# Performance work log

Measured on AMD Instinct MI355X. Metric: run time of the kernel, lower is better.

The kernel has to match this reference:

```python
import jax, jax.numpy as jnp
import numpy as np

ITEM_NUM = 100000
EMBED = 128
HIDDEN = 256
BETA = 0.5
B = 4096
H = 200

def setup_inputs() -> dict:
    key = jax.random.key(0)
    ks = jax.random.split(key, 7)
    history = jax.random.randint(ks[0], (B, H), 0, ITEM_NUM)
    target = jax.random.randint(ks[1], (B,), 0, ITEM_NUM)
    embed_history = jax.random.normal(ks[2], (ITEM_NUM, EMBED), dtype=jnp.float32) * 0.01
    embed_target = jax.random.normal(ks[3], (ITEM_NUM, EMBED), dtype=jnp.float32) * 0.01
    # nn.Linear default init: U(-1/sqrt(fan_in), 1/sqrt(fan_in)); biases zeroed by _init_weight_
    lim1 = 1.0 / np.sqrt(EMBED)
    W1 = jax.random.uniform(ks[4], (EMBED, HIDDEN), dtype=jnp.float32, minval=-lim1, maxval=lim1)
    b1 = jnp.zeros((HIDDEN,), dtype=jnp.float32)
    lim2 = 1.0 / np.sqrt(HIDDEN)
    w2 = jax.random.uniform(ks[5], (HIDDEN,), dtype=jnp.float32, minval=-lim2, maxval=lim2)
    return {"history": history, "target": target, "embed_history": embed_history,
            "embed_target": embed_target, "W1": W1, "b1": b1, "w2": w2}

def reference(history, target, embed_history, embed_target, W1, b1, w2):
    hist_e = embed_history[history]            # [B, H, d]
    tgt_e = embed_target[target][:, None, :]   # [B, 1, d]
    x = hist_e * tgt_e                          # [B, H, d]
    a = jnp.einsum('bhk,k->bh', jax.nn.relu(jnp.einsum('bhd,dk->bhk', x, W1) + b1), w2)  # [B, H]
    mask = (history != target[:, None]).astype(a.dtype)  # [B, H]
    exp_A = jnp.exp(a) * mask                  # [B, H]
    denom = jnp.sum(exp_A, axis=-1) ** BETA    # [B], beta-power normalization (not softmax)
    attn = exp_A / denom[:, None]              # [B, H]
    pred = jnp.einsum('bh,bhd,bd->b', attn, hist_e, tgt_e[:, 0, :])  # [B]
    return jax.nn.sigmoid(pred)
```

## Files before the change

kernel.cpp:

```cpp
#include <hip/hip_runtime.h>

#define B_SZ   4096
#define H_SZ   200
#define D_SZ   128
#define N_SZ   256
#define ROWS   (B_SZ * H_SZ)
#define BM     64
#define TPB    8
#define RPB    (BM * TPB)
#define NBLK   (ROWS / RPB)

typedef __attribute__((ext_vector_type(8))) short bf16x8;
typedef __attribute__((ext_vector_type(4))) float f32x4;

__device__ __forceinline__ unsigned short f2bf(float f) {
    unsigned u = __builtin_bit_cast(unsigned, f);
    u += 0x7FFFu + ((u >> 16) & 1u);
    return (unsigned short)(u >> 16);
}
__device__ __forceinline__ float bflo(unsigned d) {
    return __builtin_bit_cast(float, d << 16);
}
__device__ __forceinline__ float bfhi(unsigned d) {
    return __builtin_bit_cast(float, d & 0xFFFF0000u);
}
__device__ __forceinline__ unsigned packtr(float a, float b) {
    return (__builtin_bit_cast(unsigned, a) >> 16) |
           (__builtin_bit_cast(unsigned, b) & 0xFFFF0000u);
}

__global__ __launch_bounds__(256) void cvt_eh(const float* __restrict__ src,
                                              uint4* __restrict__ dst, int n8) {
    int i = blockIdx.x * 256 + threadIdx.x;
    if (i >= n8) return;
    const f32x4* p = (const f32x4*)src + (size_t)i * 2;
    f32x4 a = p[0], b = p[1];
    uint4 o;
    o.x = (unsigned)f2bf(a[0]) | ((unsigned)f2bf(a[1]) << 16);
    o.y = (unsigned)f2bf(a[2]) | ((unsigned)f2bf(a[3]) << 16);
    o.z = (unsigned)f2bf(b[0]) | ((unsigned)f2bf(b[1]) << 16);
    o.w = (unsigned)f2bf(b[2]) | ((unsigned)f2bf(b[3]) << 16);
    dst[i] = o;
}

__global__ __launch_bounds__(256) void cvt_w1(const float* __restrict__ src,
                                              unsigned short* __restrict__ dst) {
    int i = blockIdx.x * 256 + threadIdx.x;
    int n = i >> 7, d = i & 127;
    dst[i] = f2bf(src[d * N_SZ + n]);
}

__global__ __launch_bounds__(512, 4) void nais_main(
    const int* __restrict__ history, const int* __restrict__ target,
    const uint4* __restrict__ eh16, const float* __restrict__ et,
    const unsigned short* __restrict__ w1t, const float* __restrict__ b1,
    const float* __restrict__ w2,
    float* __restrict__ a_out, float* __restrict__ dotd_out)
{
    __shared__ uint4 AbufV[2][BM * 256 / 16];
    __shared__ float apart[2][8][BM];
    __shared__ float tgt_p[4][16][12];
    __shared__ int   tgt_i[4];

    const int tid  = threadIdx.x;
    const int wid  = tid >> 6;
    const int lane = tid & 63;
    const int lo   = lane & 15;
    const int hi   = lane >> 4;
    const int row  = tid >> 3;
    const int seg  = tid & 7;
    const int blk  = blockIdx.x;
    const int b_base = (blk * RPB) / H_SZ;

    if (tid < 4) {
        int bb = b_base + tid;
        tgt_i[tid] = target[bb < B_SZ ? bb : (B_SZ - 1)];
    }
    __syncthreads();
    {
        const int r4 = tid >> 7, d = tid & 127;
        tgt_p[r4][d >> 3][d & 7] = et[(size_t)tgt_i[r4] * D_SZ + d];
    }

    bf16x8 wfrag[4][2];
    #pragma unroll
    for (int ni = 0; ni < 2; ++ni) {
        int n = 32 * wid + 16 * ni + lo;
        #pragma unroll
        for (int ki = 0; ki < 4; ++ki)
            wfrag[ki][ni] = *(const bf16x8*)(w1t + (size_t)n * D_SZ + 32 * ki + 8 * hi);
    }
    const int n0 = 32 * wid + 4 * hi;
    const f32x4 b1a = *(const f32x4*)(b1 + n0);
    const f32x4 b1b = *(const f32x4*)(b1 + n0 + 16);
    const f32x4 w2a = *(const f32x4*)(w2 + n0);
    const f32x4 w2b = *(const f32x4*)(w2 + n0 + 16);

    const int grow0 = blk * RPB + row;
    const int* hrow = history + grow0;
    int ih_nxt = hrow[BM];
    uint4 hq0, hq1;
    {
        const uint4* p = eh16 + (size_t)hrow[0] * 16;
        hq0 = p[seg]; hq1 = p[8 + seg];
    }
    __syncthreads();

    for (int t = 0; t < TPB; ++t) {
        char* Ab = (char*)AbufV[t & 1];
        const int gr    = grow0 + t * BM;
        const int b_loc = gr / H_SZ - b_base;

        {
            const float* tA = &tgt_p[b_loc][seg][0];
            const float* tB = &tgt_p[b_loc][8 + seg][0];
            f32x4 ta0 = *(const f32x4*)tA, ta1 = *(const f32x4*)(tA + 4);
            f32x4 tb0 = *(const f32x4*)tB, tb1 = *(const f32x4*)(tB + 4);
            float tAv[8] = {ta0[0], ta0[1], ta0[2], ta0[3], ta1[0], ta1[1], ta1[2], ta1[3]};
            float tBv[8] = {tb0[0], tb0[1], tb0[2], tb0[3], tb1[0], tb1[1], tb1[2], tb1[3]};
            unsigned h1[4] = {hq0.x, hq0.y, hq0.z, hq0.w};
            unsigned h2[4] = {hq1.x, hq1.y, hq1.z, hq1.w};
            unsigned xp1[4], xp2[4];
            float s = 0.f;
            #pragma unroll
            for (int j = 0; j < 4; ++j) {
                float x0 = bflo(h1[j]) * tAv[2 * j];
                float x1 = bfhi(h1[j]) * tAv[2 * j + 1];
                float y0 = bflo(h2[j]) * tBv[2 * j];
                float y1 = bfhi(h2[j]) * tBv[2 * j + 1];
                s += (x0 + x1) + (y0 + y1);
                xp1[j] = packtr(x0, x1);
                xp2[j] = packtr(y0, y1);
            }
            s += __shfl_xor(s, 1);
            s += __shfl_xor(s, 2);
            s += __shfl_xor(s, 4);
            if (seg == 0) dotd_out[gr] = s;
            const unsigned sw = (unsigned)((row & 7) << 4);
            char* rb = Ab + row * 256;
            *(uint4*)(rb + (((unsigned)(16 * seg)) ^ sw))          = uint4{xp1[0], xp1[1], xp1[2], xp1[3]};
            *(uint4*)(rb + (128u + (((unsigned)(16 * seg)) ^ sw))) = uint4{xp2[0], xp2[1], xp2[2], xp2[3]};
        }
        __syncthreads();

        if (t + 1 < TPB) {
            int ih_cur = ih_nxt;
            if (t + 2 < TPB) ih_nxt = hrow[(t + 2) * BM];
            const uint4* p = eh16 + (size_t)ih_cur * 16;
            hq0 = p[seg]; hq1 = p[8 + seg];
        }

        if (t > 0 && tid < BM) {
            const float* ap = &apart[(t - 1) & 1][0][tid];
            float a = ap[0];
            #pragma unroll
            for (int w = 1; w < 8; ++w) a += ap[w * BM];
            a_out[blk * RPB + (t - 1) * BM + tid] = a;
        }

        #pragma unroll
        for (int mi = 0; mi < 4; ++mi) {
            const int rr = 16 * mi + lo;
            const unsigned swr = (unsigned)((rr & 7) << 4);
            bf16x8 af[4];
            #pragma unroll
            for (int ki = 0; ki < 4; ++ki) {
                unsigned off = ((unsigned)(64 * ki + 16 * hi)) ^ swr;
                af[ki] = *(const bf16x8*)(Ab + rr * 256 + off);
            }
            f32x4 acc0 = b1a;
            f32x4 acc1 = b1b;
            __builtin_amdgcn_s_setprio(1);
            #pragma unroll
            for (int ki = 0; ki < 4; ++ki) {
                acc0 = __builtin_amdgcn_mfma_f32_16x16x32_bf16(wfrag[ki][0], af[ki], acc0, 0, 0, 0);
                acc1 = __builtin_amdgcn_mfma_f32_16x16x32_bf16(wfrag[ki][1], af[ki], acc1, 0, 0, 0);
            }
            __builtin_amdgcn_s_setprio(0);
            float v = fmaxf(acc0[0], 0.f) * w2a[0] + fmaxf(acc1[0], 0.f) * w2b[0];
            v += fmaxf(acc0[1], 0.f) * w2a[1] + fmaxf(acc1[1], 0.f) * w2b[1];
            v += fmaxf(acc0[2], 0.f) * w2a[2] + fmaxf(acc1[2], 0.f) * w2b[2];
            v += fmaxf(acc0[3], 0.f) * w2a[3] + fmaxf(acc1[3], 0.f) * w2b[3];
            v += __shfl_xor(v, 16);
            v += __shfl_xor(v, 32);
            if (lane < 16) apart[t & 1][wid][16 * mi + lane] = v;
        }
    }
    __syncthreads();
    if (tid < BM) {
        const float* ap = &apart[(TPB - 1) & 1][0][tid];
        float a = ap[0];
        #pragma unroll
        for (int w = 1; w < 8; ++w) a += ap[w * BM];
        a_out[blk * RPB + (TPB - 1) * BM + tid] = a;
    }
}

__global__ __launch_bounds__(64) void nais_finish(
    const int* __restrict__ history, const int* __restrict__ target,
    const float* __restrict__ a_in, const float* __restrict__ dotd_in,
    float* __restrict__ out)
{
    const int b    = blockIdx.x;
    const int lane = threadIdx.x;
    const int tgt  = target[b];
    float s1 = 0.f, s2 = 0.f;
    for (int h = lane; h < H_SZ; h += 64) {
        int rg = b * H_SZ + h;
        float e = (history[rg] != tgt) ? __expf(a_in[rg]) : 0.f;
        s1 += e;
        s2 += e * dotd_in[rg];
    }
    #pragma unroll
    for (int o = 1; o < 64; o <<= 1) {
        s1 += __shfl_xor(s1, o);
        s2 += __shfl_xor(s2, o);
    }
    if (lane == 0) {
        float pred = s2 / sqrtf(s1);
        out[b] = 1.f / (1.f + __expf(-pred));
    }
}

extern "C" void kernel_launch(void* const* d_in, const int* in_sizes, int n_in,
                              void* d_out, int out_size, void* d_ws, size_t ws_size,
                              hipStream_t stream) {
    const int*   history = (const int*)d_in[0];
    const int*   target  = (const int*)d_in[1];
    const float* eh      = (const float*)d_in[2];
    const float* et      = (const float*)d_in[3];
    const float* W1      = (const float*)d_in[4];
    const float* b1      = (const float*)d_in[5];
    const float* w2      = (const float*)d_in[6];
    float* out = (float*)d_out;

    char* ws = (char*)d_ws;
    uint4*          eh16 = (uint4*)ws;
    unsigned short* w1t  = (unsigned short*)(ws + (size_t)100000 * D_SZ * 2);
    float*          a_ws = (float*)(ws + (size_t)100000 * D_SZ * 2 + N_SZ * D_SZ * 2);
    float*          dotd_ws = a_ws + ROWS;

    const int n8 = 100000 * D_SZ / 8;
    cvt_eh<<<(n8 + 255) / 256, 256, 0, stream>>>(eh, eh16, n8);
    cvt_w1<<<(N_SZ * D_SZ) / 256, 256, 0, stream>>>(W1, w1t);
    nais_main<<<NBLK, 512, 0, stream>>>(history, target, eh16, et, w1t, b1, w2, a_ws, dotd_ws);
    nais_finish<<<B_SZ, 64, 0, stream>>>(history, target, a_ws, dotd_ws, out);
}
```

Before: 101.5 us.

## Switch bf16 path to scaled fp16 with packed multiply and dot2

```diff
diff --git a/kernel.cpp b/kernel.cpp
--- a/kernel.cpp
+++ b/kernel.cpp
@@ -10,23 +10,15 @@
 #define RPB    (BM * TPB)
 #define NBLK   (ROWS / RPB)
 
-typedef __attribute__((ext_vector_type(8))) short bf16x8;
+typedef _Float16 f16;
+typedef __attribute__((ext_vector_type(2))) _Float16 f16x2;
+typedef __attribute__((ext_vector_type(8))) _Float16 f16x8;
 typedef __attribute__((ext_vector_type(4))) float f32x4;
 
-__device__ __forceinline__ unsigned short f2bf(float f) {
-    unsigned u = __builtin_bit_cast(unsigned, f);
-    u += 0x7FFFu + ((u >> 16) & 1u);
-    return (unsigned short)(u >> 16);
-}
-__device__ __forceinline__ float bflo(unsigned d) {
-    return __builtin_bit_cast(float, d << 16);
-}
-__device__ __forceinline__ float bfhi(unsigned d) {
-    return __builtin_bit_cast(float, d & 0xFFFF0000u);
-}
-__device__ __forceinline__ unsigned packtr(float a, float b) {
-    return (__builtin_bit_cast(unsigned, a) >> 16) |
-           (__builtin_bit_cast(unsigned, b) & 0xFFFF0000u);
+union H8 { f16x8 v; f16x2 p[4]; uint4 u; };
+
+__device__ __forceinline__ f16x2 pkrtz(float a, float b) {
+    return __builtin_bit_cast(f16x2, __builtin_amdgcn_cvt_pkrtz(a, b));
 }
 
 __global__ __launch_bounds__(256) void cvt_eh(const float* __restrict__ src,
@@ -36,30 +28,30 @@
     const f32x4* p = (const f32x4*)src + (size_t)i * 2;
     f32x4 a = p[0], b = p[1];
     uint4 o;
-    o.x = (unsigned)f2bf(a[0]) | ((unsigned)f2bf(a[1]) << 16);
-    o.y = (unsigned)f2bf(a[2]) | ((unsigned)f2bf(a[3]) << 16);
-    o.z = (unsigned)f2bf(b[0]) | ((unsigned)f2bf(b[1]) << 16);
-    o.w = (unsigned)f2bf(b[2]) | ((unsigned)f2bf(b[3]) << 16);
+    o.x = __builtin_bit_cast(unsigned, pkrtz(a[0], a[1]));
+    o.y = __builtin_bit_cast(unsigned, pkrtz(a[2], a[3]));
+    o.z = __builtin_bit_cast(unsigned, pkrtz(b[0], b[1]));
+    o.w = __builtin_bit_cast(unsigned, pkrtz(b[2], b[3]));
     dst[i] = o;
 }
 
 __global__ __launch_bounds__(256) void cvt_w1(const float* __restrict__ src,
-                                              unsigned short* __restrict__ dst) {
+                                              f16* __restrict__ dst) {
     int i = blockIdx.x * 256 + threadIdx.x;
     int n = i >> 7, d = i & 127;
-    dst[i] = f2bf(src[d * N_SZ + n]);
+    dst[i] = (f16)(src[d * N_SZ + n] * 0.0625f);
 }
 
 __global__ __launch_bounds__(512, 4) void nais_main(
     const int* __restrict__ history, const int* __restrict__ target,
-    const uint4* __restrict__ eh16, const float* __restrict__ et,
-    const unsigned short* __restrict__ w1t, const float* __restrict__ b1,
+    const uint4* __restrict__ ehh, const float* __restrict__ et,
+    const f16* __restrict__ w1t, const float* __restrict__ b1,
     const float* __restrict__ w2,
     float* __restrict__ a_out, float* __restrict__ dotd_out)
 {
     __shared__ uint4 AbufV[2][BM * 256 / 16];
     __shared__ float apart[2][8][BM];
-    __shared__ float tgt_p[4][16][12];
+    __shared__ f16   tgt_h[4][D_SZ];
     __shared__ int   tgt_i[4];
 
     const int tid  = threadIdx.x;
@@ -77,18 +69,19 @@
         tgt_i[tid] = target[bb < B_SZ ? bb : (B_SZ - 1)];
     }
     __syncthreads();
-    {
-        const int r4 = tid >> 7, d = tid & 127;
-        tgt_p[r4][d >> 3][d & 7] = et[(size_t)tgt_i[r4] * D_SZ + d];
-    }
-
-    bf16x8 wfrag[4][2];
+    if (tid < 256) {
+        const int r4 = tid >> 6, j = (tid & 63) * 2;
+        const float* src = et + (size_t)tgt_i[r4] * D_SZ + j;
+        ((f16x2*)tgt_h)[tid] = pkrtz(src[0] * 16.f, src[1] * 16.f);
+    }
+
+    f16x8 wfrag[4][2];
     #pragma unroll
     for (int ni = 0; ni < 2; ++ni) {
         int n = 32 * wid + 16 * ni + lo;
         #pragma unroll
         for (int ki = 0; ki < 4; ++ki)
-            wfrag[ki][ni] = *(const bf16x8*)(w1t + (size_t)n * D_SZ + 32 * ki + 8 * hi);
+            wfrag[ki][ni] = *(const f16x8*)(w1t + (size_t)n * D_SZ + 32 * ki + 8 * hi);
     }
     const int n0 = 32 * wid + 4 * hi;
     const f32x4 b1a = *(const f32x4*)(b1 + n0);
@@ -98,55 +91,49 @@
 
     const int grow0 = blk * RPB + row;
     const int* hrow = history + grow0;
+    int ih_cur = hrow[0];
     int ih_nxt = hrow[BM];
     uint4 hq0, hq1;
     {
-        const uint4* p = eh16 + (size_t)hrow[0] * 16;
+        const uint4* p = ehh + (size_t)ih_cur * 16;
         hq0 = p[seg]; hq1 = p[8 + seg];
     }
+    int b_loc = grow0 / H_SZ - b_base;
+    int rem   = grow0 - (b_loc + b_base) * H_SZ;
     __syncthreads();
 
     for (int t = 0; t < TPB; ++t) {
         char* Ab = (char*)AbufV[t & 1];
-        const int gr    = grow0 + t * BM;
-        const int b_loc = gr / H_SZ - b_base;
+        const int gr = grow0 + t * BM;
 
         {
-            const float* tA = &tgt_p[b_loc][seg][0];
-            const float* tB = &tgt_p[b_loc][8 + seg][0];
-            f32x4 ta0 = *(const f32x4*)tA, ta1 = *(const f32x4*)(tA + 4);
-            f32x4 tb0 = *(const f32x4*)tB, tb1 = *(const f32x4*)(tB + 4);
-            float tAv[8] = {ta0[0], ta0[1], ta0[2], ta0[3], ta1[0], ta1[1], ta1[2], ta1[3]};
-            float tBv[8] = {tb0[0], tb0[1], tb0[2], tb0[3], tb1[0], tb1[1], tb1[2], tb1[3]};
-            unsigned h1[4] = {hq0.x, hq0.y, hq0.z, hq0.w};
-            unsigned h2[4] = {hq1.x, hq1.y, hq1.z, hq1.w};
-            unsigned xp1[4], xp2[4];
+            H8 h1, h2, t1, t2, x1, x2;
+            h1.u = hq0; h2.u = hq1;
+            t1.v = *(const f16x8*)&tgt_h[b_loc][8 * seg];
+            t2.v = *(const f16x8*)&tgt_h[b_loc][64 + 8 * seg];
+            x1.v = h1.v * t1.v;
+            x2.v = h2.v * t2.v;
             float s = 0.f;
             #pragma unroll
             for (int j = 0; j < 4; ++j) {
-                float x0 = bflo(h1[j]) * tAv[2 * j];
-                float x1 = bfhi(h1[j]) * tAv[2 * j + 1];
-                float y0 = bflo(h2[j]) * tBv[2 * j];
-                float y1 = bfhi(h2[j]) * tBv[2 * j + 1];
-                s += (x0 + x1) + (y0 + y1);
-                xp1[j] = packtr(x0, x1);
-                xp2[j] = packtr(y0, y1);
+                s = __builtin_amdgcn_fdot2(h1.p[j], t1.p[j], s, false);
+                s = __builtin_amdgcn_fdot2(h2.p[j], t2.p[j], s, false);
             }
             s += __shfl_xor(s, 1);
             s += __shfl_xor(s, 2);
             s += __shfl_xor(s, 4);
-            if (seg == 0) dotd_out[gr] = s;
+            if (seg == 0) dotd_out[gr] = s * 0.0625f;
             const unsigned sw = (unsigned)((row & 7) << 4);
             char* rb = Ab + row * 256;
-            *(uint4*)(rb + (((unsigned)(16 * seg)) ^ sw))          = uint4{xp1[0], xp1[1], xp1[2], xp1[3]};
-            *(uint4*)(rb + (128u + (((unsigned)(16 * seg)) ^ sw))) = uint4{xp2[0], xp2[1], xp2[2], xp2[3]};
+            *(uint4*)(rb + (((unsigned)(16 * seg)) ^ sw))          = x1.u;
+            *(uint4*)(rb + (128u + (((unsigned)(16 * seg)) ^ sw))) = x2.u;
         }
         __syncthreads();
 
         if (t + 1 < TPB) {
-            int ih_cur = ih_nxt;
+            ih_cur = ih_nxt;
             if (t + 2 < TPB) ih_nxt = hrow[(t + 2) * BM];
-            const uint4* p = eh16 + (size_t)ih_cur * 16;
+            const uint4* p = ehh + (size_t)ih_cur * 16;
             hq0 = p[seg]; hq1 = p[8 + seg];
         }
 
@@ -162,19 +149,19 @@
         for (int mi = 0; mi < 4; ++mi) {
             const int rr = 16 * mi + lo;
             const unsigned swr = (unsigned)((rr & 7) << 4);
-            bf16x8 af[4];
+            f16x8 af[4];
             #pragma unroll
             for (int ki = 0; ki < 4; ++ki) {
                 unsigned off = ((unsigned)(64 * ki + 16 * hi)) ^ swr;
-                af[ki] = *(const bf16x8*)(Ab + rr * 256 + off);
+                af[ki] = *(const f16x8*)(Ab + rr * 256 + off);
             }
             f32x4 acc0 = b1a;
             f32x4 acc1 = b1b;
             __builtin_amdgcn_s_setprio(1);
             #pragma unroll
             for (int ki = 0; ki < 4; ++ki) {
-                acc0 = __builtin_amdgcn_mfma_f32_16x16x32_bf16(wfrag[ki][0], af[ki], acc0, 0, 0, 0);
-                acc1 = __builtin_amdgcn_mfma_f32_16x16x32_bf16(wfrag[ki][1], af[ki], acc1, 0, 0, 0);
+                acc0 = __builtin_amdgcn_mfma_f32_16x16x32_f16(wfrag[ki][0], af[ki], acc0, 0, 0, 0);
+                acc1 = __builtin_amdgcn_mfma_f32_16x16x32_f16(wfrag[ki][1], af[ki], acc1, 0, 0, 0);
             }
             __builtin_amdgcn_s_setprio(0);
             float v = fmaxf(acc0[0], 0.f) * w2a[0] + fmaxf(acc1[0], 0.f) * w2b[0];
@@ -185,6 +172,9 @@
             v += __shfl_xor(v, 32);
             if (lane < 16) apart[t & 1][wid][16 * mi + lane] = v;
         }
+
+        rem += BM;
+        if (rem >= H_SZ) { rem -= H_SZ; ++b_loc; }
     }
     __syncthreads();
     if (tid < BM) {
@@ -235,14 +225,14 @@
     float* out = (float*)d_out;
 
     char* ws = (char*)d_ws;
-    uint4*          eh16 = (uint4*)ws;
-    unsigned short* w1t  = (unsigned short*)(ws + (size_t)100000 * D_SZ * 2);
-    float*          a_ws = (float*)(ws + (size_t)100000 * D_SZ * 2 + N_SZ * D_SZ * 2);
-    float*          dotd_ws = a_ws + ROWS;
+    uint4* ehh = (uint4*)ws;
+    f16*   w1t = (f16*)(ws + (size_t)100000 * D_SZ * 2);
+    float* a_ws = (float*)(ws + (size_t)100000 * D_SZ * 2 + N_SZ * D_SZ * 2);
+    float* dotd_ws = a_ws + ROWS;
 
     const int n8 = 100000 * D_SZ / 8;
-    cvt_eh<<<(n8 + 255) / 256, 256, 0, stream>>>(eh, eh16, n8);
+    cvt_eh<<<(n8 + 255) / 256, 256, 0, stream>>>(eh, ehh, n8);
     cvt_w1<<<(N_SZ * D_SZ) / 256, 256, 0, stream>>>(W1, w1t);
-    nais_main<<<NBLK, 512, 0, stream>>>(history, target, eh16, et, w1t, b1, w2, a_ws, dotd_ws);
+    nais_main<<<NBLK, 512, 0, stream>>>(history, target, ehh, et, w1t, b1, w2, a_ws, dotd_ws);
     nais_finish<<<B_SZ, 64, 0, stream>>>(history, target, a_ws, dotd_ws, out);
 }
```

Result: faster. 98.76 us (-2.7%).

## Gather fp32 history embeddings directly and drop the bf16 table conversion pass

Applied to the files above, without the earlier changes.

```diff
diff --git a/kernel.cpp b/kernel.cpp
--- a/kernel.cpp
+++ b/kernel.cpp
@@ -11,6 +11,7 @@
 #define NBLK   (ROWS / RPB)
 
 typedef __attribute__((ext_vector_type(8))) short bf16x8;
+typedef __attribute__((ext_vector_type(2))) float f32x2;
 typedef __attribute__((ext_vector_type(4))) float f32x4;
 
 __device__ __forceinline__ unsigned short f2bf(float f) {
@@ -18,29 +19,9 @@
     u += 0x7FFFu + ((u >> 16) & 1u);
     return (unsigned short)(u >> 16);
 }
-__device__ __forceinline__ float bflo(unsigned d) {
-    return __builtin_bit_cast(float, d << 16);
-}
-__device__ __forceinline__ float bfhi(unsigned d) {
-    return __builtin_bit_cast(float, d & 0xFFFF0000u);
-}
-__device__ __forceinline__ unsigned packtr(float a, float b) {
-    return (__builtin_bit_cast(unsigned, a) >> 16) |
-           (__builtin_bit_cast(unsigned, b) & 0xFFFF0000u);
-}
-
-__global__ __launch_bounds__(256) void cvt_eh(const float* __restrict__ src,
-                                              uint4* __restrict__ dst, int n8) {
-    int i = blockIdx.x * 256 + threadIdx.x;
-    if (i >= n8) return;
-    const f32x4* p = (const f32x4*)src + (size_t)i * 2;
-    f32x4 a = p[0], b = p[1];
-    uint4 o;
-    o.x = (unsigned)f2bf(a[0]) | ((unsigned)f2bf(a[1]) << 16);
-    o.y = (unsigned)f2bf(a[2]) | ((unsigned)f2bf(a[3]) << 16);
-    o.z = (unsigned)f2bf(b[0]) | ((unsigned)f2bf(b[1]) << 16);
-    o.w = (unsigned)f2bf(b[2]) | ((unsigned)f2bf(b[3]) << 16);
-    dst[i] = o;
+__device__ __forceinline__ unsigned bfpack(f32x2 x) {
+    return __builtin_amdgcn_perm(__builtin_bit_cast(unsigned, x[1]),
+                                 __builtin_bit_cast(unsigned, x[0]), 0x07060302u);
 }
 
 __global__ __launch_bounds__(256) void cvt_w1(const float* __restrict__ src,
@@ -52,14 +33,14 @@
 
 __global__ __launch_bounds__(512, 4) void nais_main(
     const int* __restrict__ history, const int* __restrict__ target,
-    const uint4* __restrict__ eh16, const float* __restrict__ et,
+    const float* __restrict__ eh, const float* __restrict__ et,
     const unsigned short* __restrict__ w1t, const float* __restrict__ b1,
     const float* __restrict__ w2,
     float* __restrict__ a_out, float* __restrict__ dotd_out)
 {
     __shared__ uint4 AbufV[2][BM * 256 / 16];
     __shared__ float apart[2][8][BM];
-    __shared__ float tgt_p[4][16][12];
+    __shared__ float tgt_f[4][D_SZ];
     __shared__ int   tgt_i[4];
 
     const int tid  = threadIdx.x;
@@ -79,7 +60,7 @@
     __syncthreads();
     {
         const int r4 = tid >> 7, d = tid & 127;
-        tgt_p[r4][d >> 3][d & 7] = et[(size_t)tgt_i[r4] * D_SZ + d];
+        tgt_f[r4][d] = et[(size_t)tgt_i[r4] * D_SZ + d];
     }
 
     bf16x8 wfrag[4][2];
@@ -98,56 +79,54 @@
 
     const int grow0 = blk * RPB + row;
     const int* hrow = history + grow0;
+    int ih_cur = hrow[0];
     int ih_nxt = hrow[BM];
-    uint4 hq0, hq1;
+    f32x4 hq0, hq1, hq2, hq3;
     {
-        const uint4* p = eh16 + (size_t)hrow[0] * 16;
-        hq0 = p[seg]; hq1 = p[8 + seg];
-    }
+        const f32x4* p = (const f32x4*)(eh + (size_t)ih_cur * D_SZ + 16 * seg);
+        hq0 = p[0]; hq1 = p[1]; hq2 = p[2]; hq3 = p[3];
+    }
+    int b_loc = grow0 / H_SZ - b_base;
+    int rem   = grow0 - (b_loc + b_base) * H_SZ;
     __syncthreads();
 
     for (int t = 0; t < TPB; ++t) {
         char* Ab = (char*)AbufV[t & 1];
-        const int gr    = grow0 + t * BM;
-        const int b_loc = gr / H_SZ - b_base;
+        const int gr = grow0 + t * BM;
 
         {
-            const float* tA = &tgt_p[b_loc][seg][0];
-            const float* tB = &tgt_p[b_loc][8 + seg][0];
-            f32x4 ta0 = *(const f32x4*)tA, ta1 = *(const f32x4*)(tA + 4);
-            f32x4 tb0 = *(const f32x4*)tB, tb1 = *(const f32x4*)(tB + 4);
-            float tAv[8] = {ta0[0], ta0[1], ta0[2], ta0[3], ta1[0], ta1[1], ta1[2], ta1[3]};
-            float tBv[8] = {tb0[0], tb0[1], tb0[2], tb0[3], tb1[0], tb1[1], tb1[2], tb1[3]};
-            unsigned h1[4] = {hq0.x, hq0.y, hq0.z, hq0.w};
-            unsigned h2[4] = {hq1.x, hq1.y, hq1.z, hq1.w};
-            unsigned xp1[4], xp2[4];
-            float s = 0.f;
-            #pragma unroll
-            for (int j = 0; j < 4; ++j) {
-                float x0 = bflo(h1[j]) * tAv[2 * j];
-                float x1 = bfhi(h1[j]) * tAv[2 * j + 1];
-                float y0 = bflo(h2[j]) * tBv[2 * j];
-                float y1 = bfhi(h2[j]) * tBv[2 * j + 1];
-                s += (x0 + x1) + (y0 + y1);
-                xp1[j] = packtr(x0, x1);
-                xp2[j] = packtr(y0, y1);
-            }
+            const f32x2* tp = (const f32x2*)&tgt_f[b_loc][16 * seg];
+            f32x2 h[8];
+            h[0] = f32x2{hq0[0], hq0[1]}; h[1] = f32x2{hq0[2], hq0[3]};
+            h[2] = f32x2{hq1[0], hq1[1]}; h[3] = f32x2{hq1[2], hq1[3]};
+            h[4] = f32x2{hq2[0], hq2[1]}; h[5] = f32x2{hq2[2], hq2[3]};
+            h[6] = f32x2{hq3[0], hq3[1]}; h[7] = f32x2{hq3[2], hq3[3]};
+            f32x2 x[8];
+            #pragma unroll
+            for (int j = 0; j < 8; ++j) x[j] = h[j] * tp[j];
+            f32x2 acc01 = x[0] + x[1], acc23 = x[2] + x[3];
+            f32x2 acc45 = x[4] + x[5], acc67 = x[6] + x[7];
+            f32x2 accA = acc01 + acc23, accB = acc45 + acc67;
+            f32x2 accT = accA + accB;
+            float s = accT[0] + accT[1];
             s += __shfl_xor(s, 1);
             s += __shfl_xor(s, 2);
             s += __shfl_xor(s, 4);
             if (seg == 0) dotd_out[gr] = s;
+            uint4 o1 = uint4{bfpack(x[0]), bfpack(x[1]), bfpack(x[2]), bfpack(x[3])};
+            uint4 o2 = uint4{bfpack(x[4]), bfpack(x[5]), bfpack(x[6]), bfpack(x[7])};
             const unsigned sw = (unsigned)((row & 7) << 4);
             char* rb = Ab + row * 256;
-            *(uint4*)(rb + (((unsigned)(16 * seg)) ^ sw))          = uint4{xp1[0], xp1[1], xp1[2], xp1[3]};
-            *(uint4*)(rb + (128u + (((unsigned)(16 * seg)) ^ sw))) = uint4{xp2[0], xp2[1], xp2[2], xp2[3]};
+            *(uint4*)(rb + (((unsigned)(32 * seg)) ^ sw))      = o1;
+            *(uint4*)(rb + (((unsigned)(32 * seg + 16)) ^ sw)) = o2;
         }
         __syncthreads();
 
         if (t + 1 < TPB) {
-            int ih_cur = ih_nxt;
+            ih_cur = ih_nxt;
             if (t + 2 < TPB) ih_nxt = hrow[(t + 2) * BM];
-            const uint4* p = eh16 + (size_t)ih_cur * 16;
-            hq0 = p[seg]; hq1 = p[8 + seg];
+            const f32x4* p = (const f32x4*)(eh + (size_t)ih_cur * D_SZ + 16 * seg);
+            hq0 = p[0]; hq1 = p[1]; hq2 = p[2]; hq3 = p[3];
         }
 
         if (t > 0 && tid < BM) {
@@ -185,6 +164,9 @@
             v += __shfl_xor(v, 32);
             if (lane < 16) apart[t & 1][wid][16 * mi + lane] = v;
         }
+
+        rem += BM;
+        if (rem >= H_SZ) { rem -= H_SZ; ++b_loc; }
     }
     __syncthreads();
     if (tid < BM) {
@@ -235,14 +217,11 @@
     float* out = (float*)d_out;
 
     char* ws = (char*)d_ws;
-    uint4*          eh16 = (uint4*)ws;
-    unsigned short* w1t  = (unsigned short*)(ws + (size_t)100000 * D_SZ * 2);
-    float*          a_ws = (float*)(ws + (size_t)100000 * D_SZ * 2 + N_SZ * D_SZ * 2);
-    float*          dotd_ws = a_ws + ROWS;
-
-    const int n8 = 100000 * D_SZ / 8;
-    cvt_eh<<<(n8 + 255) / 256, 256, 0, stream>>>(eh, eh16, n8);
+    unsigned short* w1t = (unsigned short*)ws;
+    float* a_ws    = (float*)(ws + N_SZ * D_SZ * 2);
+    float* dotd_ws = a_ws + ROWS;
+
     cvt_w1<<<(N_SZ * D_SZ) / 256, 256, 0, stream>>>(W1, w1t);
-    nais_main<<<NBLK, 512, 0, stream>>>(history, target, eh16, et, w1t, b1, w2, a_ws, dotd_ws);
+    nais_main<<<NBLK, 512, 0, stream>>>(history, target, eh, et, w1t, b1, w2, a_ws, dotd_ws);
     nais_finish<<<B_SZ, 64, 0, stream>>>(history, target, a_ws, dotd_ws, out);
 }
```

Measured after the change: 96.87 us. 4.6% less time.
